# Kernel optimization log

Measured on AMD Instinct MI355X. Metric: run time of the kernel, lower is better.

The kernel has to match this reference:

```python
import jax, jax.numpy as jnp
import numpy as np

N_RAYS = 131072
N_SAMPLES = 128
FEAT_DIM = 3
FAR_DELTA = 1e10  # sentinel delta appended for the last sample, as in the torch code


def setup_inputs() -> dict:
    key = jax.random.key(0)
    k1, k2, k3 = jax.random.split(key, 3)
    # densities are non-negative (output of e.g. relu/softplus in NeRF)
    density = jax.random.uniform(k1, (N_RAYS, N_SAMPLES), dtype=jnp.float32) * 2.0
    feature = jax.random.uniform(k2, (N_RAYS, N_SAMPLES, FEAT_DIM), dtype=jnp.float32)
    # monotonically increasing per-ray sample depths: near + cumsum(uniform bins)
    bins = jax.random.uniform(k3, (N_RAYS, N_SAMPLES), dtype=jnp.float32) * 0.05 + 0.01
    depth_values = 1.0 + jnp.cumsum(bins, axis=1)
    return {"density": density, "feature": feature, "depth_values": depth_values}


def reference(density, feature, depth_values):
    # deltas: consecutive depth differences, with a huge last delta (torch.cat(..., 1e10*ones))
    deltas = jnp.concatenate(
        [depth_values[:, 1:] - depth_values[:, :-1],
         jnp.full_like(depth_values[:, :1], FAR_DELTA)],
        axis=-1,
    )  # [N, S]
    att = jnp.exp(-density * deltas)              # exp(-sigma_i * delta_i), [N, S]
    # inclusive prefix product, matching the loop: T[i] = T[i-1]*exp(-sigma_i*delta_i)
    T = jnp.cumprod(att, axis=1)                  # [N, S]
    weights = T * (1.0 - att)                     # [N, S]
    feat_out = jnp.einsum("ns,nsc->nc", weights, feature)      # [N, 3]
    depth_out = jnp.sum(weights * depth_values, axis=1)         # [N]
    return feat_out, depth_out
```

## Files before the change

### kernel.cpp

```cpp
#include <hip/hip_runtime.h>

#define N_RAYS    131072
#define N_SAMPLES 128
#define FAR_DELTA 1e10f

__global__ __launch_bounds__(256) void VolumeRenderer_57612691308835_kernel(
    const float* __restrict__ density,
    const float* __restrict__ feature,
    const float* __restrict__ depth,
    float* __restrict__ out_feat,
    float* __restrict__ out_depth)
{
    const int wave = threadIdx.x >> 6;
    const int lane = threadIdx.x & 63;
    const int ray  = (blockIdx.x << 2) + wave;
    if (ray >= N_RAYS) return;

    const int  s0   = lane << 1;
    const long base = (long)ray * N_SAMPLES;

    const float2 den = *(const float2*)(density + base + s0);
    const float2 dep = *(const float2*)(depth   + base + s0);
    const float* fp  = feature + (base + s0) * 3;
    const float2 f01 = *(const float2*)(fp);
    const float2 f23 = *(const float2*)(fp + 2);
    const float2 f45 = *(const float2*)(fp + 4);

    const float d_next = __shfl_down(dep.x, 1);
    const float delta0 = dep.y - dep.x;
    const float delta1 = (lane == 63) ? FAR_DELTA : (d_next - dep.y);

    const float att0 = __expf(-den.x * delta0);
    const float att1 = __expf(-den.y * delta1);

    float scan = att0 * att1;
    #pragma unroll
    for (int off = 1; off < 64; off <<= 1) {
        const float v = __shfl_up(scan, off);
        scan *= (lane >= off) ? v : 1.0f;
    }
    float excl = __shfl_up(scan, 1);
    if (lane == 0) excl = 1.0f;

    const float T0 = excl * att0;
    const float T1 = T0   * att1;
    const float w0 = T0 * (1.0f - att0);
    const float w1 = T1 * (1.0f - att1);

    float fx = w0 * f01.x + w1 * f23.y;
    float fy = w0 * f01.y + w1 * f45.x;
    float fz = w0 * f23.x + w1 * f45.y;
    float dd = w0 * dep.x + w1 * dep.y;

    #pragma unroll
    for (int off = 32; off >= 1; off >>= 1) {
        fx += __shfl_xor(fx, off);
        fy += __shfl_xor(fy, off);
        fz += __shfl_xor(fz, off);
        dd += __shfl_xor(dd, off);
    }

    if (lane == 0) {
        out_feat[ray * 3 + 0] = fx;
        out_feat[ray * 3 + 1] = fy;
        out_feat[ray * 3 + 2] = fz;
        out_depth[ray]        = dd;
    }
}

extern "C" void kernel_launch(void* const* d_in, const int* in_sizes, int n_in,
                              void* d_out, int out_size, void* d_ws, size_t ws_size,
                              hipStream_t stream) {
    const float* density = (const float*)d_in[0];
    const float* feature = (const float*)d_in[1];
    const float* depth   = (const float*)d_in[2];

    float* out_feat  = (float*)d_out;
    float* out_depth = (float*)d_out + (long)N_RAYS * 3;

    const int rays_per_block = 4;
    const int grid = N_RAYS / rays_per_block;
    VolumeRenderer_57612691308835_kernel<<<grid, 256, 0, stream>>>(
        density, feature, depth, out_feat, out_depth);
}
```

Measured before the change: 349.9 us.

## Map each ray to 16 lanes with 8 samples and DPP row scans

Each ray is now handled by a 16-lane DPP row instead of a full wave, with each lane loading 8 samples via float4 vector loads. The prefix-product scan and the reductions use row-local DPP shifts in place of ds_bpermute shuffles, and a transpose-style quad permutation finishes the four sums so lanes 0-3 each write one output. This cuts cross-lane communication and widens memory accesses, and the block covers 16 rays instead of 4. In exchange each lane holds more registers and does a longer serial chain of exp and multiply work.

```diff
diff --git a/kernel.cpp b/kernel.cpp
--- a/kernel.cpp
+++ b/kernel.cpp
@@ -3,6 +3,16 @@
 #define N_RAYS    131072
 #define N_SAMPLES 128
 #define FAR_DELTA 1e10f
+
+#define ROW_SHL(n) (0x100 + (n))
+#define ROW_SHR(n) (0x110 + (n))
+#define QPERM(a,b,c,d) ((a) | ((b) << 2) | ((c) << 4) | ((d) << 6))
+
+template <int CTRL>
+__device__ __forceinline__ float dpp_f(float v, float ident) {
+    return __int_as_float(__builtin_amdgcn_update_dpp(
+        __float_as_int(ident), __float_as_int(v), CTRL, 0xF, 0xF, false));
+}
 
 __global__ __launch_bounds__(256) void VolumeRenderer_57612691308835_kernel(
     const float* __restrict__ density,
@@ -11,61 +21,79 @@
     float* __restrict__ out_feat,
     float* __restrict__ out_depth)
 {
-    const int wave = threadIdx.x >> 6;
-    const int lane = threadIdx.x & 63;
-    const int ray  = (blockIdx.x << 2) + wave;
-    if (ray >= N_RAYS) return;
+    const int tid  = threadIdx.x;
+    const int wave = tid >> 6;
+    const int lane = tid & 63;
+    const int p    = lane & 15;
+    const int g    = lane >> 4;
+    const int ray  = (blockIdx.x << 4) + (wave << 2) + g;
 
-    const int  s0   = lane << 1;
-    const long base = (long)ray * N_SAMPLES;
+    const long base = (long)ray * N_SAMPLES + p * 8;
 
-    const float2 den = *(const float2*)(density + base + s0);
-    const float2 dep = *(const float2*)(depth   + base + s0);
-    const float* fp  = feature + (base + s0) * 3;
-    const float2 f01 = *(const float2*)(fp);
-    const float2 f23 = *(const float2*)(fp + 2);
-    const float2 f45 = *(const float2*)(fp + 4);
+    const float4 dn0 = *(const float4*)(density + base);
+    const float4 dn1 = *(const float4*)(density + base + 4);
+    const float4 dp0 = *(const float4*)(depth + base);
+    const float4 dp1 = *(const float4*)(depth + base + 4);
+    const float4* fp = (const float4*)(feature + base * 3);
+    const float4 f0 = fp[0], f1 = fp[1], f2 = fp[2];
+    const float4 f3 = fp[3], f4 = fp[4], f5 = fp[5];
 
-    const float d_next = __shfl_down(dep.x, 1);
-    const float delta0 = dep.y - dep.x;
-    const float delta1 = (lane == 63) ? FAR_DELTA : (d_next - dep.y);
+    const float dnext = dpp_f<ROW_SHL(1)>(dp0.x, 0.0f);
+    const float d7 = (p == 15) ? FAR_DELTA : (dnext - dp1.w);
 
-    const float att0 = __expf(-den.x * delta0);
-    const float att1 = __expf(-den.y * delta1);
+    const float a0 = __expf(-dn0.x * (dp0.y - dp0.x));
+    const float a1 = __expf(-dn0.y * (dp0.z - dp0.y));
+    const float a2 = __expf(-dn0.z * (dp0.w - dp0.z));
+    const float a3 = __expf(-dn0.w * (dp1.x - dp0.w));
+    const float a4 = __expf(-dn1.x * (dp1.y - dp1.x));
+    const float a5 = __expf(-dn1.y * (dp1.z - dp1.y));
+    const float a6 = __expf(-dn1.z * (dp1.w - dp1.z));
+    const float a7 = __expf(-dn1.w * d7);
 
-    float scan = att0 * att1;
-    #pragma unroll
-    for (int off = 1; off < 64; off <<= 1) {
-        const float v = __shfl_up(scan, off);
-        scan *= (lane >= off) ? v : 1.0f;
-    }
-    float excl = __shfl_up(scan, 1);
-    if (lane == 0) excl = 1.0f;
+    float s = ((a0 * a1) * (a2 * a3)) * ((a4 * a5) * (a6 * a7));
+    s *= dpp_f<ROW_SHR(1)>(s, 1.0f);
+    s *= dpp_f<ROW_SHR(2)>(s, 1.0f);
+    s *= dpp_f<ROW_SHR(4)>(s, 1.0f);
+    s *= dpp_f<ROW_SHR(8)>(s, 1.0f);
+    float T = dpp_f<ROW_SHR(1)>(s, 1.0f);
 
-    const float T0 = excl * att0;
-    const float T1 = T0   * att1;
-    const float w0 = T0 * (1.0f - att0);
-    const float w1 = T1 * (1.0f - att1);
+    T *= a0; const float w0 = T * (1.0f - a0);
+    T *= a1; const float w1 = T * (1.0f - a1);
+    T *= a2; const float w2 = T * (1.0f - a2);
+    T *= a3; const float w3 = T * (1.0f - a3);
+    T *= a4; const float w4 = T * (1.0f - a4);
+    T *= a5; const float w5 = T * (1.0f - a5);
+    T *= a6; const float w6 = T * (1.0f - a6);
+    T *= a7; const float w7 = T * (1.0f - a7);
 
-    float fx = w0 * f01.x + w1 * f23.y;
-    float fy = w0 * f01.y + w1 * f45.x;
-    float fz = w0 * f23.x + w1 * f45.y;
-    float dd = w0 * dep.x + w1 * dep.y;
+    float fx = w0*f0.x + w1*f0.w + w2*f1.z + w3*f2.y + w4*f3.x + w5*f3.w + w6*f4.z + w7*f5.y;
+    float fy = w0*f0.y + w1*f1.x + w2*f1.w + w3*f2.z + w4*f3.y + w5*f4.x + w6*f4.w + w7*f5.z;
+    float fz = w0*f0.z + w1*f1.y + w2*f2.x + w3*f2.w + w4*f3.z + w5*f4.y + w6*f5.x + w7*f5.w;
+    float dd = w0*dp0.x + w1*dp0.y + w2*dp0.z + w3*dp0.w + w4*dp1.x + w5*dp1.y + w6*dp1.z + w7*dp1.w;
 
-    #pragma unroll
-    for (int off = 32; off >= 1; off >>= 1) {
-        fx += __shfl_xor(fx, off);
-        fy += __shfl_xor(fy, off);
-        fz += __shfl_xor(fz, off);
-        dd += __shfl_xor(dd, off);
-    }
+    fx += dpp_f<ROW_SHL(8)>(fx, 0.0f);
+    fy += dpp_f<ROW_SHL(8)>(fy, 0.0f);
+    fz += dpp_f<ROW_SHL(8)>(fz, 0.0f);
+    dd += dpp_f<ROW_SHL(8)>(dd, 0.0f);
+    fx += dpp_f<ROW_SHL(4)>(fx, 0.0f);
+    fy += dpp_f<ROW_SHL(4)>(fy, 0.0f);
+    fz += dpp_f<ROW_SHL(4)>(fz, 0.0f);
+    dd += dpp_f<ROW_SHL(4)>(dd, 0.0f);
 
-    if (lane == 0) {
-        out_feat[ray * 3 + 0] = fx;
-        out_feat[ray * 3 + 1] = fy;
-        out_feat[ray * 3 + 2] = fz;
-        out_depth[ray]        = dd;
-    }
+    const bool o1 = (p & 1);
+    const float sA = o1 ? fx : fy;
+    const float rA = dpp_f<QPERM(1, 0, 3, 2)>(sA, 0.0f);
+    if (o1) fy += rA; else fx += rA;
+    const float sB = o1 ? fz : dd;
+    const float rB = dpp_f<QPERM(1, 0, 3, 2)>(sB, 0.0f);
+    if (o1) dd += rB; else fz += rB;
+    const float own = (p & 2) ? (o1 ? dd : fz) : (o1 ? fy : fx);
+    const float sC  = (p & 2) ? (o1 ? fy : fx) : (o1 ? dd : fz);
+    const float rC  = dpp_f<QPERM(2, 3, 0, 1)>(sC, 0.0f);
+    const float res = own + rC;
+
+    if (p < 3)       out_feat[(long)ray * 3 + p] = res;
+    else if (p == 3) out_depth[ray] = res;
 }
 
 extern "C" void kernel_launch(void* const* d_in, const int* in_sizes, int n_in,
@@ -78,7 +106,7 @@
     float* out_feat  = (float*)d_out;
     float* out_depth = (float*)d_out + (long)N_RAYS * 3;
 
-    const int rays_per_block = 4;
+    const int rays_per_block = 16;
     const int grid = N_RAYS / rays_per_block;
     VolumeRenderer_57612691308835_kernel<<<grid, 256, 0, stream>>>(
         density, feature, depth, out_feat, out_depth);
```

After: 352.1 us. About the same (+0.6%).
